# Optimization experiments

Measured on AMD Instinct MI355X. Metric: run time of the kernel, lower is better.

The kernel has to match this reference:

```python
import jax, jax.numpy as jnp
import numpy as np

N_ORDER = 64
SEQ_LEN = 4096
BATCH = 256


def _hippo_scale_buffers(N: int, L: int):
    """Build bilinear-discretized scaled-Legendre (HiPPO-LegS) transition buffers."""
    q = np.arange(N, dtype=np.float64)
    col, row = np.meshgrid(q, q)  # col[i,j]=j, row[i,j]=i
    r = 2 * q + 1
    M = -(np.where(row >= col, r, 0) - np.diag(q))
    T = np.sqrt(np.diag(2 * q + 1))
    A = T @ M @ np.linalg.inv(T)              # (N,N) continuous-time A
    Bv = np.sqrt(2 * q + 1)                   # diag(T) -> continuous-time B vector
    t = np.arange(1, L + 1, dtype=np.float64)
    A_sc = A[None, :, :] / t[:, None, None]   # (L,N,N)
    B_sc = Bv[None, :] / t[:, None]           # (L,N)
    I = np.eye(N, dtype=np.float64)
    Mm = I[None] - 0.5 * A_sc
    Nn = I[None] + 0.5 * A_sc
    A_d = np.linalg.solve(Mm, Nn)                        # (L,N,N)
    B_d = np.linalg.solve(Mm, B_sc[..., None])[..., 0]   # (L,N)
    return A_d.astype(np.float32), B_d.astype(np.float32)


def setup_inputs() -> dict:
    key = jax.random.key(0)
    inputs = jax.random.normal(key, (SEQ_LEN, BATCH), dtype=jnp.float32)
    A_np, B_np = _hippo_scale_buffers(N_ORDER, SEQ_LEN)
    return {
        "inputs": inputs,
        "A_stacked": jnp.asarray(A_np),   # (L,N,N)
        "B_stacked": jnp.asarray(B_np),   # (L,N)
    }


def reference(inputs, A_stacked, B_stacked):
    """x_t = A_t @ x_{t-1} + B_t * inputs_t, x_{-1} = 0. Returns (L, B, N)."""
    L = inputs.shape[0]
    # u[t, b, :] = inputs[t, b] * B_stacked[t, :]
    u = inputs[..., None] * B_stacked[:L, None, :]  # (L,B,N)

    def step(x, au):
        A_t, u_t = au                                  # (N,N), (B,N)
        x = u_t + jnp.einsum('ij,bj->bi', A_t, x)      # (B,N)
        return x, x

    x0 = jnp.zeros(u.shape[1:], dtype=u.dtype)
    _, xs = jax.lax.scan(step, x0, (A_stacked[:L], u))
    return xs  # (L,B,N)
```

## Files before the change

### kernel.cpp

```cpp
#include <hip/hip_runtime.h>
#include <cstdint>


#define TID ((int)threadIdx.x)

typedef _Float16 half8 __attribute__((ext_vector_type(8)));
typedef _Float16 half4v __attribute__((ext_vector_type(4)));
typedef float f32x4 __attribute__((ext_vector_type(4)));

constexpr int SUBL  = 16;
constexpr int PAD   = 68;

constexpr size_t WS_W = 0;
constexpr size_t WS_Q = 262144;
constexpr size_t WS_P = WS_Q + 1048576;
constexpr size_t WS_Z = WS_P + 262144;
constexpr size_t WS_H = WS_Z + 1048576;
constexpr size_t OLD_WS_FLOATS = WS_H + 1048576;

constexpr int SLOT   = 20480;
constexpr int APITCH = 144;
constexpr int AL_OFF = 9216;
constexpr int BV_OFF = 18432;
constexpr int U_OFF  = 18688;
constexpr size_t AWS_BYTES = (size_t)4096 * SLOT;

__device__ __forceinline__ void stage64x64(const float* __restrict__ g, float* __restrict__ l) {
#pragma unroll
  for (int r = 0; r < 4; ++r) {
    int id = TID + 256 * r;
    int i = id >> 4, j0 = (id & 15) << 2;
    *reinterpret_cast<float4*>(&l[i * PAD + j0]) =
        *reinterpret_cast<const float4*>(&g[i * 64 + j0]);
  }
}

__device__ __forceinline__ void matmul_tile(const float* __restrict__ Ml,
                                            const float* __restrict__ Al,
                                            float* __restrict__ Dl,
                                            int i_lo, int i_hi) {
  float acc[4][4];
#pragma unroll
  for (int a = 0; a < 4; ++a)
#pragma unroll
    for (int b = 0; b < 4; ++b) acc[a][b] = 0.f;
  const int j0 = i_hi << 2;
#pragma unroll
  for (int kq = 0; kq < 16; ++kq) {
    const int k0 = kq << 2;
    float4 mf[4], af[4];
#pragma unroll
    for (int a = 0; a < 4; ++a)
      mf[a] = *reinterpret_cast<const float4*>(&Ml[(i_lo + 16 * a) * PAD + k0]);
#pragma unroll
    for (int kk = 0; kk < 4; ++kk)
      af[kk] = *reinterpret_cast<const float4*>(&Al[(k0 + kk) * PAD + j0]);
#pragma unroll
    for (int a = 0; a < 4; ++a) {
      acc[a][0] += mf[a].x * af[0].x + mf[a].y * af[1].x + mf[a].z * af[2].x + mf[a].w * af[3].x;
      acc[a][1] += mf[a].x * af[0].y + mf[a].y * af[1].y + mf[a].z * af[2].y + mf[a].w * af[3].y;
      acc[a][2] += mf[a].x * af[0].z + mf[a].y * af[1].z + mf[a].z * af[2].z + mf[a].w * af[3].z;
      acc[a][3] += mf[a].x * af[0].w + mf[a].y * af[1].w + mf[a].z * af[2].w + mf[a].w * af[3].w;
    }
  }
#pragma unroll
  for (int a = 0; a < 4; ++a)
    *reinterpret_cast<float4*>(&Dl[(i_lo + 16 * a) * PAD + j0]) =
        make_float4(acc[a][0], acc[a][1], acc[a][2], acc[a][3]);
}

__global__ __launch_bounds__(256) void k1_fused(const float* __restrict__ Ag,
                                                const float* __restrict__ Bg,
                                                const float* __restrict__ inp,
                                                unsigned char* __restrict__ Aws,
                                                float* __restrict__ W,
                                                float* __restrict__ Qw) {
  __shared__ float Ms[2][64 * PAD];
  __shared__ float As[2][64 * PAD];
  __shared__ float Bvs[2][64];
  const int c = blockIdx.x;
  const int i_lo = TID & 15, i_hi = TID >> 4;
  const int r_i0 = TID >> 4;
  const int r_j0 = (TID & 15) << 2;

  for (int idx = TID; idx < 64 * PAD; idx += 256) Ms[0][idx] = 0.f;

  float4 pc[4];
  float4 bvc = make_float4(0.f, 0.f, 0.f, 0.f);
  {
    const float* g = Ag + (size_t)(c * SUBL + SUBL - 1) * 4096;
#pragma unroll
    for (int r = 0; r < 4; ++r)
      pc[r] = *reinterpret_cast<const float4*>(&g[(r_i0 + 16 * r) * 64 + r_j0]);
    if (TID < 16)
      bvc = *reinterpret_cast<const float4*>(&Bg[(size_t)(c * SUBL + SUBL - 1) * 64 + TID * 4]);
  }
  __syncthreads();
  if (TID < 64) Ms[0][TID * PAD + TID] = 1.f;
#pragma unroll
  for (int r = 0; r < 4; ++r)
    *reinterpret_cast<float4*>(&As[0][(r_i0 + 16 * r) * PAD + r_j0]) = pc[r];
  if (TID < 16) *reinterpret_cast<float4*>(&Bvs[0][TID * 4]) = bvc;
  __syncthreads();

  int cur = 0, ab = 0;
  for (int k = SUBL - 1; k >= 0; --k) {
    const int t = c * SUBL + k;
    unsigned char* slot = Aws + (size_t)t * SLOT;
    float4 pn[4];
    float4 bvn = make_float4(0.f, 0.f, 0.f, 0.f);
    if (k > 0) {
      const float* g = Ag + (size_t)(t - 1) * 4096;
#pragma unroll
      for (int r = 0; r < 4; ++r)
        pn[r] = *reinterpret_cast<const float4*>(&g[(r_i0 + 16 * r) * 64 + r_j0]);
      if (TID < 16)
        bvn = *reinterpret_cast<const float4*>(&Bg[(size_t)(t - 1) * 64 + TID * 4]);
    }
    if (TID >= 64 && TID < 128) {
      int q = TID - 64;
      *reinterpret_cast<float4*>(slot + U_OFF + q * 16) =
          *reinterpret_cast<const float4*>(inp + (size_t)t * 256 + q * 4);
    }
    if (TID < 16) *reinterpret_cast<float4*>(slot + BV_OFF + TID * 16) = bvc;
    if (TID < 64) {
      float wv = 0.f;
#pragma unroll
      for (int kq = 0; kq < 16; ++kq) {
        float4 m = *reinterpret_cast<const float4*>(&Ms[cur][TID * PAD + kq * 4]);
        float4 b = *reinterpret_cast<const float4*>(&Bvs[ab][kq * 4]);
        wv += m.x * b.x + m.y * b.y + m.z * b.z + m.w * b.w;
      }
      W[t * 64 + TID] = wv;
    }
#pragma unroll
    for (int r = 0; r < 4; ++r) {
      float vv[4] = {pc[r].x, pc[r].y, pc[r].z, pc[r].w};
      half4v hh, ll;
#pragma unroll
      for (int e = 0; e < 4; ++e) {
        _Float16 h = (_Float16)vv[e];
        hh[e] = h;
        ll[e] = (_Float16)(vv[e] - (float)h);
      }
      const int row = r_i0 + 16 * r;
      *reinterpret_cast<half4v*>(slot + row * APITCH + r_j0 * 2) = hh;
      *reinterpret_cast<half4v*>(slot + AL_OFF + row * APITCH + r_j0 * 2) = ll;
    }
    if (TID < 64) {
      half8 z = {};
      *reinterpret_cast<half8*>(slot + TID * APITCH + 128) = z;
      *reinterpret_cast<half8*>(slot + AL_OFF + TID * APITCH + 128) = z;
    }
    matmul_tile(Ms[cur], As[ab], Ms[cur ^ 1], i_lo, i_hi);
    if (k > 0) {
#pragma unroll
      for (int r = 0; r < 4; ++r)
        *reinterpret_cast<float4*>(&As[ab ^ 1][(r_i0 + 16 * r) * PAD + r_j0]) = pn[r];
      if (TID < 16) *reinterpret_cast<float4*>(&Bvs[ab ^ 1][TID * 4]) = bvn;
#pragma unroll
      for (int r = 0; r < 4; ++r) pc[r] = pn[r];
      bvc = bvn;
    }
    __syncthreads();
    cur ^= 1;
    ab ^= 1;
  }
#pragma unroll
  for (int r = 0; r < 4; ++r) {
    int id = TID + 256 * r;
    int i = id >> 4, j0 = (id & 15) << 2;
    *reinterpret_cast<float4*>(&Qw[(size_t)c * 4096 + i * 64 + j0]) =
        *reinterpret_cast<const float4*>(&Ms[cur][i * PAD + j0]);
  }
}

__global__ __launch_bounds__(256) void k1_suffix(const float* __restrict__ Ag,
                                                 const float* __restrict__ Bg,
                                                 float* __restrict__ W,
                                                 float* __restrict__ Qw) {
  __shared__ float Ms[2][64 * PAD];
  __shared__ float As[64 * PAD];
  __shared__ float Bvs[64];
  const int c = blockIdx.x;
  const int i_lo = TID & 15, i_hi = TID >> 4;
  for (int idx = TID; idx < 64 * PAD; idx += 256) Ms[0][idx] = 0.f;
  __syncthreads();
  if (TID < 64) Ms[0][TID * PAD + TID] = 1.f;
  int cur = 0;
  for (int k = SUBL - 1; k >= 0; --k) {
    const int t = c * SUBL + k;
    stage64x64(Ag + (size_t)t * 4096, As);
    if (TID < 16)
      *reinterpret_cast<float4*>(&Bvs[TID * 4]) =
          *reinterpret_cast<const float4*>(&Bg[t * 64 + TID * 4]);
    __syncthreads();
    if (TID < 64) {
      float wv = 0.f;
#pragma unroll
      for (int kq = 0; kq < 16; ++kq) {
        float4 m = *reinterpret_cast<const float4*>(&Ms[cur][TID * PAD + kq * 4]);
        float4 b = *reinterpret_cast<const float4*>(&Bvs[kq * 4]);
        wv += m.x * b.x + m.y * b.y + m.z * b.z + m.w * b.w;
      }
      W[t * 64 + TID] = wv;
    }
    matmul_tile(Ms[cur], As, Ms[cur ^ 1], i_lo, i_hi);
    __syncthreads();
    cur ^= 1;
  }
#pragma unroll
  for (int r = 0; r < 4; ++r) {
    int id = TID + 256 * r;
    int i = id >> 4, j0 = (id & 15) << 2;
    *reinterpret_cast<float4*>(&Qw[(size_t)c * 4096 + i * 64 + j0]) =
        *reinterpret_cast<const float4*>(&Ms[cur][i * PAD + j0]);
  }
}

__global__ __launch_bounds__(256) void k1b_combine(const float* __restrict__ Qw,
                                                   float* __restrict__ W,
                                                   float* __restrict__ Pw) {
  __shared__ float R[2][64 * PAD];
  __shared__ float Qs[64 * PAD];
  __shared__ float wm[16 * PAD];
  const int s = blockIdx.x;
  const int i_lo = TID & 15, i_hi = TID >> 4;
  int cur = 0;
  for (int m = 3; m >= 0; --m) {
    const int c = 4 * s + m;
    stage64x64(Qw + (size_t)c * 4096, Qs);
    {
      int tt = TID >> 4, i0 = (TID & 15) << 2;
      *reinterpret_cast<float4*>(&wm[tt * PAD + i0]) =
          *reinterpret_cast<const float4*>(&W[(size_t)(c * 16 + tt) * 64 + i0]);
    }
    __syncthreads();
    if (m < 3) {
      float acc[4] = {0.f, 0.f, 0.f, 0.f};
#pragma unroll
      for (int kq = 0; kq < 16; ++kq) {
        const int k0 = kq << 2;
        float4 wf = *reinterpret_cast<const float4*>(&wm[i_hi * PAD + k0]);
#pragma unroll
        for (int a = 0; a < 4; ++a) {
          float4 rf = *reinterpret_cast<const float4*>(&R[cur][(i_lo + 16 * a) * PAD + k0]);
          acc[a] += rf.x * wf.x + rf.y * wf.y + rf.z * wf.z + rf.w * wf.w;
        }
      }
#pragma unroll
      for (int a = 0; a < 4; ++a)
        W[(size_t)(c * 16 + i_hi) * 64 + i_lo + 16 * a] = acc[a];
      matmul_tile(R[cur], Qs, R[cur ^ 1], i_lo, i_hi);
    } else {
#pragma unroll
      for (int r = 0; r < 4; ++r) {
        int id = TID + 256 * r;
        int i = id >> 4, j0 = (id & 15) << 2;
        *reinterpret_cast<float4*>(&R[cur ^ 1][i * PAD + j0]) =
            *reinterpret_cast<const float4*>(&Qs[i * PAD + j0]);
      }
    }
    __syncthreads();
    cur ^= 1;
  }
#pragma unroll
  for (int r = 0; r < 4; ++r) {
    int id = TID + 256 * r;
    int i = id >> 4, j0 = (id & 15) << 2;
    *reinterpret_cast<float4*>(&Pw[(size_t)s * 4096 + i * 64 + j0]) =
        *reinterpret_cast<const float4*>(&R[cur][i * PAD + j0]);
  }
}

__global__ __launch_bounds__(256) void k1c_zgemm(const float* __restrict__ inp,
                                                 const float* __restrict__ W,
                                                 float* __restrict__ Zw) {
  __shared__ float inT[64 * PAD];
  __shared__ float wm[64 * PAD];
  const int s = blockIdx.x >> 2, g = blockIdx.x & 3;
  const int b0 = 64 * g, t0 = s * 64;
  const int i_lo = TID & 15, i_hi = TID >> 4;
#pragma unroll
  for (int r = 0; r < 4; ++r) {
    int id = TID + 256 * r;
    int tl = id >> 4, b4 = (id & 15) << 2;
    float4 v = *reinterpret_cast<const float4*>(&inp[(size_t)(t0 + tl) * 256 + b0 + b4]);
    inT[(b4 + 0) * PAD + tl] = v.x;
    inT[(b4 + 1) * PAD + tl] = v.y;
    inT[(b4 + 2) * PAD + tl] = v.z;
    inT[(b4 + 3) * PAD + tl] = v.w;
  }
#pragma unroll
  for (int r = 0; r < 4; ++r) {
    int id = TID + 256 * r;
    int tl = id >> 4, i0 = (id & 15) << 2;
    *reinterpret_cast<float4*>(&wm[tl * PAD + i0]) =
        *reinterpret_cast<const float4*>(&W[(size_t)(t0 + tl) * 64 + i0]);
  }
  __syncthreads();
  float acc[4][4];
#pragma unroll
  for (int a = 0; a < 4; ++a)
#pragma unroll
    for (int q = 0; q < 4; ++q) acc[a][q] = 0.f;
  const int j0c = i_hi << 2;
#pragma unroll
  for (int kq = 0; kq < 16; ++kq) {
    const int k0 = kq << 2;
    float4 bf[4], wf[4];
#pragma unroll
    for (int a = 0; a < 4; ++a)
      bf[a] = *reinterpret_cast<const float4*>(&inT[(i_lo + 16 * a) * PAD + k0]);
#pragma unroll
    for (int kk = 0; kk < 4; ++kk)
      wf[kk] = *reinterpret_cast<const float4*>(&wm[(k0 + kk) * PAD + j0c]);
#pragma unroll
    for (int a = 0; a < 4; ++a) {
      acc[a][0] += bf[a].x * wf[0].x + bf[a].y * wf[1].x + bf[a].z * wf[2].x + bf[a].w * wf[3].x;
      acc[a][1] += bf[a].x * wf[0].y + bf[a].y * wf[1].y + bf[a].z * wf[2].y + bf[a].w * wf[3].y;
      acc[a][2] += bf[a].x * wf[0].z + bf[a].y * wf[1].z + bf[a].z * wf[2].z + bf[a].w * wf[3].z;
      acc[a][3] += bf[a].x * wf[0].w + bf[a].y * wf[1].w + bf[a].z * wf[2].w + bf[a].w * wf[3].w;
    }
  }
  __syncthreads();
#pragma unroll
  for (int a = 0; a < 4; ++a)
    *reinterpret_cast<float4*>(&wm[(i_lo + 16 * a) * PAD + j0c]) =
        make_float4(acc[a][0], acc[a][1], acc[a][2], acc[a][3]);
  __syncthreads();
#pragma unroll
  for (int r = 0; r < 4; ++r) {
    int id = TID + 256 * r;
    int bl = id >> 4, i0 = (id & 15) << 2;
    *reinterpret_cast<float4*>(&Zw[(size_t)s * 16384 + (b0 + bl) * 64 + i0]) =
        *reinterpret_cast<const float4*>(&wm[bl * PAD + i0]);
  }
}

__global__ __launch_bounds__(256) void k2_carry(const float* __restrict__ Pw,
                                                const float* __restrict__ Zw,
                                                float* __restrict__ Hw) {
  __shared__ float Pt[2][64 * PAD];
  __shared__ float xb[2][4 * PAD];
  const int g = blockIdx.x;
  const int bl = TID >> 6, i = TID & 63;
  const int bg = 4 * g + bl;
  const int ir = TID >> 4, j0 = (TID & 15) << 2;
  for (int idx = TID; idx < 4 * PAD; idx += 256) xb[0][idx] = 0.f;
  float4 p0[4];
#pragma unroll
  for (int r = 0; r < 4; ++r)
    p0[r] = *reinterpret_cast<const float4*>(&Pw[(ir + 16 * r) * 64 + j0]);
  float zc = Zw[(size_t)bg * 64 + i];
#pragma unroll
  for (int r = 0; r < 4; ++r) {
    int row = ir + 16 * r;
    Pt[0][(j0 + 0) * PAD + row] = p0[r].x;
    Pt[0][(j0 + 1) * PAD + row] = p0[r].y;
    Pt[0][(j0 + 2) * PAD + row] = p0[r].z;
    Pt[0][(j0 + 3) * PAD + row] = p0[r].w;
  }
  __syncthreads();
  float h = 0.f;
  for (int s = 0; s < 64; ++s) {
    const int rb = s & 1, wb = rb ^ 1;
    float4 pn[4];
    float zn = 0.f;
    if (s < 63) {
#pragma unroll
      for (int r = 0; r < 4; ++r)
        pn[r] = *reinterpret_cast<const float4*>(
            &Pw[(size_t)(s + 1) * 4096 + (ir + 16 * r) * 64 + j0]);
      zn = Zw[(size_t)(s + 1) * 16384 + bg * 64 + i];
    }
    Hw[(size_t)s * 16384 + bg * 64 + i] = h;
    float acc = zc;
#pragma unroll
    for (int jq = 0; jq < 16; ++jq) {
      const int jj = jq << 2;
      float4 xf = *reinterpret_cast<const float4*>(&xb[rb][bl * PAD + jj]);
      acc += Pt[rb][(jj + 0) * PAD + i] * xf.x + Pt[rb][(jj + 1) * PAD + i] * xf.y +
             Pt[rb][(jj + 2) * PAD + i] * xf.z + Pt[rb][(jj + 3) * PAD + i] * xf.w;
    }
    h = acc;
    xb[wb][bl * PAD + i] = h;
    if (s < 63) {
#pragma unroll
      for (int r = 0; r < 4; ++r) {
        int row = ir + 16 * r;
        Pt[wb][(j0 + 0) * PAD + row] = pn[r].x;
        Pt[wb][(j0 + 1) * PAD + row] = pn[r].y;
        Pt[wb][(j0 + 2) * PAD + row] = pn[r].z;
        Pt[wb][(j0 + 3) * PAD + row] = pn[r].w;
      }
      zc = zn;
    }
    __syncthreads();
  }
}

__global__ __launch_bounds__(256) void k3_final(const float* __restrict__ Ag,
                                                const float* __restrict__ Bg,
                                                const float* __restrict__ inp,
                                                const float* __restrict__ Hw,
                                                float* __restrict__ out) {
  __shared__ float As[64 * PAD];
  __shared__ float xs[64 * PAD];
  __shared__ float Bvs[64];
  __shared__ float ins[64];
  const int s = blockIdx.x >> 2, g = blockIdx.x & 3;
  const int b0 = 64 * g;
  const int i_lo = TID & 15, i_hi = TID >> 4;
#pragma unroll
  for (int r = 0; r < 4; ++r) {
    int id = TID + 256 * r;
    int bl = id >> 4, i0 = (id & 15) << 2;
    *reinterpret_cast<float4*>(&xs[bl * PAD + i0]) =
        *reinterpret_cast<const float4*>(&Hw[(size_t)s * 16384 + (b0 + bl) * 64 + i0]);
  }
  for (int k = 0; k < 64; ++k) {
    const int t = s * 64 + k;
    stage64x64(Ag + (size_t)t * 4096, As);
    if (TID < 16)
      *reinterpret_cast<float4*>(&Bvs[TID * 4]) =
          *reinterpret_cast<const float4*>(&Bg[t * 64 + TID * 4]);
    if (TID >= 64 && TID < 80) {
      int q = TID - 64;
      *reinterpret_cast<float4*>(&ins[q * 4]) =
          *reinterpret_cast<const float4*>(&inp[(size_t)t * 256 + b0 + q * 4]);
    }
    __syncthreads();
    float acc[4][4];
#pragma unroll
    for (int a = 0; a < 4; ++a)
#pragma unroll
      for (int r = 0; r < 4; ++r) acc[a][r] = 0.f;
#pragma unroll
    for (int jq = 0; jq < 16; ++jq) {
      const int j0 = jq << 2;
      float4 af[4], xf[4];
#pragma unroll
      for (int a = 0; a < 4; ++a)
        af[a] = *reinterpret_cast<const float4*>(&As[(i_lo + 16 * a) * PAD + j0]);
#pragma unroll
      for (int r = 0; r < 4; ++r)
        xf[r] = *reinterpret_cast<const float4*>(&xs[(i_hi + 16 * r) * PAD + j0]);
#pragma unroll
      for (int a = 0; a < 4; ++a)
#pragma unroll
        for (int r = 0; r < 4; ++r)
          acc[a][r] += af[a].x * xf[r].x + af[a].y * xf[r].y + af[a].z * xf[r].z + af[a].w * xf[r].w;
    }
    float bv[4], ui[4];
#pragma unroll
    for (int a = 0; a < 4; ++a) bv[a] = Bvs[i_lo + 16 * a];
#pragma unroll
    for (int r = 0; r < 4; ++r) ui[r] = ins[i_hi + 16 * r];
#pragma unroll
    for (int a = 0; a < 4; ++a)
#pragma unroll
      for (int r = 0; r < 4; ++r) acc[a][r] += bv[a] * ui[r];
    __syncthreads();
#pragma unroll
    for (int r = 0; r < 4; ++r)
#pragma unroll
      for (int a = 0; a < 4; ++a)
        xs[(i_hi + 16 * r) * PAD + i_lo + 16 * a] = acc[a][r];
    __syncthreads();
#pragma unroll
    for (int r = 0; r < 4; ++r) {
      int id = TID + 256 * r;
      int bl = id >> 4, i0 = (id & 15) << 2;
      *reinterpret_cast<float4*>(&out[((size_t)t * 256 + b0 + bl) * 64 + i0]) =
          *reinterpret_cast<const float4*>(&xs[bl * PAD + i0]);
    }
  }
}

__device__ __forceinline__ void gload_lds16(const void* g, void* l) {
  __builtin_amdgcn_global_load_lds(
      (const __attribute__((address_space(1))) unsigned int*)g,
      (__attribute__((address_space(3))) unsigned int*)l, 16, 0, 0);
}

constexpr int XROWS  = 32;
constexpr int XHALF  = XROWS * APITCH;
constexpr int XBUF   = 2 * XHALF;
constexpr int LDS_X0 = 3 * SLOT;
constexpr int LDS_SZ = LDS_X0 + 2 * XBUF;

__global__ __launch_bounds__(256, 2) void k3_mfma(const unsigned char* __restrict__ Aws,
                                                  const float* __restrict__ Hw,
                                                  float* __restrict__ out) {
  __shared__ __align__(16) unsigned char sm[LDS_SZ];
  const int blk = blockIdx.x;
  const int s = (blk & 7) | ((blk >> 6) << 3);
  const int g = (blk >> 3) & 7;
  const int b0 = g << 5;
  const int lane = TID & 63, wave = TID >> 6;
  const int lm = lane & 15, quad = lane >> 4;
  const int wm = wave >> 1, wn = wave & 1;

#pragma unroll
  for (int r = 0; r < 2; ++r) {
    int id = TID + (r << 8);
    int bl = id >> 4, j0 = (id & 15) << 2;
    float4 v = *reinterpret_cast<const float4*>(
        &Hw[(size_t)s * 16384 + (size_t)(b0 + bl) * 64 + j0]);
    float vv[4] = {v.x, v.y, v.z, v.w};
    half4v hh, ll;
#pragma unroll
    for (int e = 0; e < 4; ++e) {
      _Float16 h = (_Float16)vv[e];
      hh[e] = h;
      ll[e] = (_Float16)(vv[e] - (float)h);
    }
    *reinterpret_cast<half4v*>(sm + LDS_X0 + bl * APITCH + (j0 << 1)) = hh;
    *reinterpret_cast<half4v*>(sm + LDS_X0 + XHALF + bl * APITCH + (j0 << 1)) = ll;
  }

  const size_t t0 = (size_t)s * 64;
#pragma unroll
  for (int sl = 0; sl < 2; ++sl) {
    const unsigned char* gsl = Aws + (t0 + sl) * SLOT;
#pragma unroll
    for (int r = 0; r < 5; ++r) {
      int off = ((r << 2) + wave) << 10;
      gload_lds16(gsl + off + lane * 16, sm + sl * SLOT + off);
    }
  }

  int aoff[2][2], xoff[2], woff[2];
#pragma unroll
  for (int mt = 0; mt < 2; ++mt)
#pragma unroll
    for (int kt = 0; kt < 2; ++kt)
      aoff[mt][kt] = ((wm << 5) + (mt << 4) + lm) * APITCH + (((kt << 5) + (quad << 3)) << 1);
#pragma unroll
  for (int kt = 0; kt < 2; ++kt)
    xoff[kt] = ((wn << 4) + lm) * APITCH + (((kt << 5) + (quad << 3)) << 1);
#pragma unroll
  for (int mt = 0; mt < 2; ++mt)
    woff[mt] = ((wn << 4) + lm) * APITCH + (((wm << 5) + (mt << 4) + (quad << 2)) << 1);

  asm volatile("s_waitcnt vmcnt(5) lgkmcnt(0)" ::: "memory");
  __builtin_amdgcn_s_barrier();
  __builtin_amdgcn_sched_barrier(0);

  int bufA = 0;
  int xr = 0;
#pragma unroll 1
  for (int k = 0; k < 64; ++k) {
    const unsigned char* ab = sm + bufA * SLOT;
    if (k < 62) {
      int nb = bufA + 2; if (nb >= 3) nb -= 3;
      const unsigned char* gsl = Aws + (t0 + k + 2) * SLOT;
      unsigned char* lb = sm + nb * SLOT;
#pragma unroll
      for (int r = 0; r < 5; ++r) {
        int off = ((r << 2) + wave) << 10;
        gload_lds16(gsl + off + lane * 16, lb + off);
      }
    }
    const unsigned char* xb = sm + LDS_X0 + xr * XBUF;
    half8 fa[2][2], fal[2][2], fxh[2], fxl[2];
#pragma unroll
    for (int mt = 0; mt < 2; ++mt)
#pragma unroll
      for (int kt = 0; kt < 2; ++kt) {
        fa[mt][kt]  = *reinterpret_cast<const half8*>(ab + aoff[mt][kt]);
        fal[mt][kt] = *reinterpret_cast<const half8*>(ab + AL_OFF + aoff[mt][kt]);
      }
#pragma unroll
    for (int kt = 0; kt < 2; ++kt) {
      fxh[kt] = *reinterpret_cast<const half8*>(xb + xoff[kt]);
      fxl[kt] = *reinterpret_cast<const half8*>(xb + XHALF + xoff[kt]);
    }
    float4 bv[2];
#pragma unroll
    for (int mt = 0; mt < 2; ++mt)
      bv[mt] = *reinterpret_cast<const float4*>(
          ab + BV_OFF + (((wm << 5) + (mt << 4) + (quad << 2)) << 2));
    float uu = *reinterpret_cast<const float*>(
        ab + U_OFF + ((b0 + (wn << 4) + lm) << 2));

    f32x4 acc[2] = {};
    __builtin_amdgcn_s_setprio(1);
#pragma unroll
    for (int mt = 0; mt < 2; ++mt)
#pragma unroll
      for (int kt = 0; kt < 2; ++kt) {
        acc[mt] = __builtin_amdgcn_mfma_f32_16x16x32_f16(fa[mt][kt],  fxh[kt], acc[mt], 0, 0, 0);
        acc[mt] = __builtin_amdgcn_mfma_f32_16x16x32_f16(fal[mt][kt], fxh[kt], acc[mt], 0, 0, 0);
        acc[mt] = __builtin_amdgcn_mfma_f32_16x16x32_f16(fa[mt][kt],  fxl[kt], acc[mt], 0, 0, 0);
      }
    __builtin_amdgcn_s_setprio(0);
#pragma unroll
    for (int mt = 0; mt < 2; ++mt) {
      const float* bp = reinterpret_cast<const float*>(&bv[mt]);
#pragma unroll
      for (int e = 0; e < 4; ++e) acc[mt][e] += bp[e] * uu;
    }
    unsigned char* xw = sm + LDS_X0 + (xr ^ 1) * XBUF;
#pragma unroll
    for (int mt = 0; mt < 2; ++mt) {
      half4v hh, ll;
#pragma unroll
      for (int e = 0; e < 4; ++e) {
        float x = acc[mt][e];
        _Float16 h = (_Float16)x;
        hh[e] = h;
        ll[e] = (_Float16)(x - (float)h);
      }
      *reinterpret_cast<half4v*>(xw + woff[mt]) = hh;
      *reinterpret_cast<half4v*>(xw + XHALF + woff[mt]) = ll;
      const int bglob = b0 + (wn << 4) + lm;
      const int irow = (wm << 5) + (mt << 4) + (quad << 2);
      *reinterpret_cast<float4*>(&out[(((t0 + k) << 8) + bglob) * 64 + irow]) =
          make_float4(acc[mt][0], acc[mt][1], acc[mt][2], acc[mt][3]);
    }
    if (k < 63) {
      if (k == 0)      asm volatile("s_waitcnt vmcnt(7) lgkmcnt(0)" ::: "memory");
      else if (k < 62) asm volatile("s_waitcnt vmcnt(9) lgkmcnt(0)" ::: "memory");
      else             asm volatile("s_waitcnt vmcnt(4) lgkmcnt(0)" ::: "memory");
      __builtin_amdgcn_s_barrier();
      __builtin_amdgcn_sched_barrier(0);
    }
    bufA = (bufA + 1 == 3) ? 0 : bufA + 1;
    xr ^= 1;
  }
}

extern "C" void kernel_launch(void* const* d_in, const int* in_sizes, int n_in,
                              void* d_out, int out_size, void* d_ws, size_t ws_size,
                              hipStream_t stream) {
  const float* inputs = (const float*)d_in[0];
  const float* Ag     = (const float*)d_in[1];
  const float* Bg     = (const float*)d_in[2];
  float* out = (float*)d_out;

  const bool use_mfma = ws_size >= AWS_BYTES + OLD_WS_FLOATS * 4;
  unsigned char* Aws = (unsigned char*)d_ws;
  float* ws = (float*)((char*)d_ws + (use_mfma ? AWS_BYTES : 0));
  float* W  = ws + WS_W;
  float* Qw = ws + WS_Q;
  float* Pw = ws + WS_P;
  float* Zw = ws + WS_Z;
  float* Hw = ws + WS_H;

  if (use_mfma)
    k1_fused<<<256, 256, 0, stream>>>(Ag, Bg, inputs, Aws, W, Qw);
  else
    k1_suffix<<<256, 256, 0, stream>>>(Ag, Bg, W, Qw);
  k1b_combine<<<64, 256, 0, stream>>>(Qw, W, Pw);
  k1c_zgemm<<<256, 256, 0, stream>>>(inputs, W, Zw);
  k2_carry<<<64, 256, 0, stream>>>(Pw, Zw, Hw);
  if (use_mfma)
    k3_mfma<<<512, 256, 0, stream>>>(Aws, Hw, out);
  else
    k3_final<<<256, 256, 0, stream>>>(Ag, Bg, inputs, Hw, out);
}
```

Measured before the change: 585.1 us.

## Halve sub-chunk length to 8 and fuse combine with Z-GEMM kernel

The first-stage chunk length drops from 16 to 8 steps, so k1 launches 512 blocks instead of 256 and each block runs a shorter serial suffix-product chain. The combine kernel now folds 8 sub-chunks per 64-step block. It keeps the resulting W rows in shared memory and computes the Z GEMM for all four batch groups itself, which removes one launch and a global round trip of W. In exchange the combine stage does twice as many serial 64x64 matmuls over only 64 blocks, the Q workspace doubles, and the Z GEMM runs on 64 blocks instead of 256.

```diff
diff --git a/kernel.cpp b/kernel.cpp
--- a/kernel.cpp
+++ b/kernel.cpp
@@ -8,15 +8,16 @@
 typedef _Float16 half4v __attribute__((ext_vector_type(4)));
 typedef float f32x4 __attribute__((ext_vector_type(4)));
 
-constexpr int SUBL  = 16;
+constexpr int SUBL  = 8;
+constexpr int NSUB  = 512;
 constexpr int PAD   = 68;
 
 constexpr size_t WS_W = 0;
 constexpr size_t WS_Q = 262144;
-constexpr size_t WS_P = WS_Q + 1048576;
+constexpr size_t WS_P = WS_Q + 2097152;
 constexpr size_t WS_Z = WS_P + 262144;
 constexpr size_t WS_H = WS_Z + 1048576;
-constexpr size_t OLD_WS_FLOATS = WS_H + 1048576;
+constexpr size_t WS_TOT_FLOATS = WS_H + 1048576;
 
 constexpr int SLOT   = 20480;
 constexpr int APITCH = 144;
@@ -218,40 +219,42 @@
   }
 }
 
-__global__ __launch_bounds__(256) void k1b_combine(const float* __restrict__ Qw,
-                                                   float* __restrict__ W,
-                                                   float* __restrict__ Pw) {
+__global__ __launch_bounds__(256) void k1bc(const float* __restrict__ Qw,
+                                            const float* __restrict__ W,
+                                            const float* __restrict__ inp,
+                                            float* __restrict__ Pw,
+                                            float* __restrict__ Zw) {
   __shared__ float R[2][64 * PAD];
   __shared__ float Qs[64 * PAD];
-  __shared__ float wm[16 * PAD];
+  __shared__ float Wall[64 * PAD];
   const int s = blockIdx.x;
   const int i_lo = TID & 15, i_hi = TID >> 4;
   int cur = 0;
-  for (int m = 3; m >= 0; --m) {
-    const int c = 4 * s + m;
+  for (int m = 7; m >= 0; --m) {
+    const int c = 8 * s + m;
     stage64x64(Qw + (size_t)c * 4096, Qs);
-    {
+    if (TID < 128) {
       int tt = TID >> 4, i0 = (TID & 15) << 2;
-      *reinterpret_cast<float4*>(&wm[tt * PAD + i0]) =
-          *reinterpret_cast<const float4*>(&W[(size_t)(c * 16 + tt) * 64 + i0]);
-    }
-    __syncthreads();
-    if (m < 3) {
-      float acc[4] = {0.f, 0.f, 0.f, 0.f};
+      *reinterpret_cast<float4*>(&Wall[(m * 8 + tt) * PAD + i0]) =
+          *reinterpret_cast<const float4*>(&W[(size_t)(c * 8 + tt) * 64 + i0]);
+    }
+    __syncthreads();
+    if (m < 7) {
+      const int th = TID >> 5, ib = TID & 31;
+      float a0 = 0.f, a1 = 0.f;
 #pragma unroll
       for (int kq = 0; kq < 16; ++kq) {
         const int k0 = kq << 2;
-        float4 wf = *reinterpret_cast<const float4*>(&wm[i_hi * PAD + k0]);
-#pragma unroll
-        for (int a = 0; a < 4; ++a) {
-          float4 rf = *reinterpret_cast<const float4*>(&R[cur][(i_lo + 16 * a) * PAD + k0]);
-          acc[a] += rf.x * wf.x + rf.y * wf.y + rf.z * wf.z + rf.w * wf.w;
-        }
-      }
-#pragma unroll
-      for (int a = 0; a < 4; ++a)
-        W[(size_t)(c * 16 + i_hi) * 64 + i_lo + 16 * a] = acc[a];
+        float4 wf = *reinterpret_cast<const float4*>(&Wall[(m * 8 + th) * PAD + k0]);
+        float4 r0 = *reinterpret_cast<const float4*>(&R[cur][ib * PAD + k0]);
+        float4 r1 = *reinterpret_cast<const float4*>(&R[cur][(ib + 32) * PAD + k0]);
+        a0 += r0.x * wf.x + r0.y * wf.y + r0.z * wf.z + r0.w * wf.w;
+        a1 += r1.x * wf.x + r1.y * wf.y + r1.z * wf.z + r1.w * wf.w;
+      }
       matmul_tile(R[cur], Qs, R[cur ^ 1], i_lo, i_hi);
+      __syncthreads();
+      Wall[(m * 8 + th) * PAD + ib] = a0;
+      Wall[(m * 8 + th) * PAD + ib + 32] = a1;
     } else {
 #pragma unroll
       for (int r = 0; r < 4; ++r) {
@@ -271,70 +274,58 @@
     *reinterpret_cast<float4*>(&Pw[(size_t)s * 4096 + i * 64 + j0]) =
         *reinterpret_cast<const float4*>(&R[cur][i * PAD + j0]);
   }
-}
-
-__global__ __launch_bounds__(256) void k1c_zgemm(const float* __restrict__ inp,
-                                                 const float* __restrict__ W,
-                                                 float* __restrict__ Zw) {
-  __shared__ float inT[64 * PAD];
-  __shared__ float wm[64 * PAD];
-  const int s = blockIdx.x >> 2, g = blockIdx.x & 3;
-  const int b0 = 64 * g, t0 = s * 64;
-  const int i_lo = TID & 15, i_hi = TID >> 4;
-#pragma unroll
-  for (int r = 0; r < 4; ++r) {
-    int id = TID + 256 * r;
-    int tl = id >> 4, b4 = (id & 15) << 2;
-    float4 v = *reinterpret_cast<const float4*>(&inp[(size_t)(t0 + tl) * 256 + b0 + b4]);
-    inT[(b4 + 0) * PAD + tl] = v.x;
-    inT[(b4 + 1) * PAD + tl] = v.y;
-    inT[(b4 + 2) * PAD + tl] = v.z;
-    inT[(b4 + 3) * PAD + tl] = v.w;
-  }
-#pragma unroll
-  for (int r = 0; r < 4; ++r) {
-    int id = TID + 256 * r;
-    int tl = id >> 4, i0 = (id & 15) << 2;
-    *reinterpret_cast<float4*>(&wm[tl * PAD + i0]) =
-        *reinterpret_cast<const float4*>(&W[(size_t)(t0 + tl) * 64 + i0]);
-  }
   __syncthreads();
-  float acc[4][4];
-#pragma unroll
-  for (int a = 0; a < 4; ++a)
-#pragma unroll
-    for (int q = 0; q < 4; ++q) acc[a][q] = 0.f;
+  const int t0 = s * 64;
   const int j0c = i_hi << 2;
-#pragma unroll
-  for (int kq = 0; kq < 16; ++kq) {
-    const int k0 = kq << 2;
-    float4 bf[4], wf[4];
+  for (int g = 0; g < 4; ++g) {
+    const int b0 = 64 * g;
+#pragma unroll
+    for (int r = 0; r < 4; ++r) {
+      int id = TID + 256 * r;
+      int tl = id >> 4, b4 = (id & 15) << 2;
+      float4 v = *reinterpret_cast<const float4*>(&inp[(size_t)(t0 + tl) * 256 + b0 + b4]);
+      Qs[(b4 + 0) * PAD + tl] = v.x;
+      Qs[(b4 + 1) * PAD + tl] = v.y;
+      Qs[(b4 + 2) * PAD + tl] = v.z;
+      Qs[(b4 + 3) * PAD + tl] = v.w;
+    }
+    __syncthreads();
+    float acc[4][4];
 #pragma unroll
     for (int a = 0; a < 4; ++a)
-      bf[a] = *reinterpret_cast<const float4*>(&inT[(i_lo + 16 * a) * PAD + k0]);
-#pragma unroll
-    for (int kk = 0; kk < 4; ++kk)
-      wf[kk] = *reinterpret_cast<const float4*>(&wm[(k0 + kk) * PAD + j0c]);
-#pragma unroll
-    for (int a = 0; a < 4; ++a) {
-      acc[a][0] += bf[a].x * wf[0].x + bf[a].y * wf[1].x + bf[a].z * wf[2].x + bf[a].w * wf[3].x;
-      acc[a][1] += bf[a].x * wf[0].y + bf[a].y * wf[1].y + bf[a].z * wf[2].y + bf[a].w * wf[3].y;
-      acc[a][2] += bf[a].x * wf[0].z + bf[a].y * wf[1].z + bf[a].z * wf[2].z + bf[a].w * wf[3].z;
-      acc[a][3] += bf[a].x * wf[0].w + bf[a].y * wf[1].w + bf[a].z * wf[2].w + bf[a].w * wf[3].w;
-    }
-  }
-  __syncthreads();
-#pragma unroll
-  for (int a = 0; a < 4; ++a)
-    *reinterpret_cast<float4*>(&wm[(i_lo + 16 * a) * PAD + j0c]) =
-        make_float4(acc[a][0], acc[a][1], acc[a][2], acc[a][3]);
-  __syncthreads();
-#pragma unroll
-  for (int r = 0; r < 4; ++r) {
-    int id = TID + 256 * r;
-    int bl = id >> 4, i0 = (id & 15) << 2;
-    *reinterpret_cast<float4*>(&Zw[(size_t)s * 16384 + (b0 + bl) * 64 + i0]) =
-        *reinterpret_cast<const float4*>(&wm[bl * PAD + i0]);
+#pragma unroll
+      for (int q = 0; q < 4; ++q) acc[a][q] = 0.f;
+#pragma unroll
+    for (int kq = 0; kq < 16; ++kq) {
+      const int k0 = kq << 2;
+      float4 bf[4], wf[4];
+#pragma unroll
+      for (int a = 0; a < 4; ++a)
+        bf[a] = *reinterpret_cast<const float4*>(&Qs[(i_lo + 16 * a) * PAD + k0]);
+#pragma unroll
+      for (int kk = 0; kk < 4; ++kk)
+        wf[kk] = *reinterpret_cast<const float4*>(&Wall[(k0 + kk) * PAD + j0c]);
+#pragma unroll
+      for (int a = 0; a < 4; ++a) {
+        acc[a][0] += bf[a].x * wf[0].x + bf[a].y * wf[1].x + bf[a].z * wf[2].x + bf[a].w * wf[3].x;
+        acc[a][1] += bf[a].x * wf[0].y + bf[a].y * wf[1].y + bf[a].z * wf[2].y + bf[a].w * wf[3].y;
+        acc[a][2] += bf[a].x * wf[0].z + bf[a].y * wf[1].z + bf[a].z * wf[2].z + bf[a].w * wf[3].z;
+        acc[a][3] += bf[a].x * wf[0].w + bf[a].y * wf[1].w + bf[a].z * wf[2].w + bf[a].w * wf[3].w;
+      }
+    }
+    __syncthreads();
+#pragma unroll
+    for (int a = 0; a < 4; ++a)
+      *reinterpret_cast<float4*>(&R[0][(i_lo + 16 * a) * PAD + j0c]) =
+          make_float4(acc[a][0], acc[a][1], acc[a][2], acc[a][3]);
+    __syncthreads();
+#pragma unroll
+    for (int r = 0; r < 4; ++r) {
+      int id = TID + 256 * r;
+      int bl = id >> 4, i0 = (id & 15) << 2;
+      *reinterpret_cast<float4*>(&Zw[(size_t)s * 16384 + (b0 + bl) * 64 + i0]) =
+          *reinterpret_cast<const float4*>(&R[0][bl * PAD + i0]);
+    }
   }
 }
 
@@ -640,7 +631,7 @@
   const float* Bg     = (const float*)d_in[2];
   float* out = (float*)d_out;
 
-  const bool use_mfma = ws_size >= AWS_BYTES + OLD_WS_FLOATS * 4;
+  const bool use_mfma = ws_size >= AWS_BYTES + WS_TOT_FLOATS * 4;
   unsigned char* Aws = (unsigned char*)d_ws;
   float* ws = (float*)((char*)d_ws + (use_mfma ? AWS_BYTES : 0));
   float* W  = ws + WS_W;
@@ -650,11 +641,10 @@
   float* Hw = ws + WS_H;
 
   if (use_mfma)
-    k1_fused<<<256, 256, 0, stream>>>(Ag, Bg, inputs, Aws, W, Qw);
+    k1_fused<<<NSUB, 256, 0, stream>>>(Ag, Bg, inputs, Aws, W, Qw);
   else
-    k1_suffix<<<256, 256, 0, stream>>>(Ag, Bg, W, Qw);
-  k1b_combine<<<64, 256, 0, stream>>>(Qw, W, Pw);
-  k1c_zgemm<<<256, 256, 0, stream>>>(inputs, W, Zw);
+    k1_suffix<<<NSUB, 256, 0, stream>>>(Ag, Bg, W, Qw);
+  k1bc<<<64, 256, 0, stream>>>(Qw, W, inputs, Pw, Zw);
   k2_carry<<<64, 256, 0, stream>>>(Pw, Zw, Hw);
   if (use_mfma)
     k3_mfma<<<512, 256, 0, stream>>>(Aws, Hw, out);
```

After: 575.4 us. About the same (-1.7%).
